# Performance work log

Hardware: AMD Instinct MI355X
Metric: run time of the kernel (lower is better)

The kernel has to match this reference:

```python
import jax, jax.numpy as jnp
import numpy as np

D_MODEL = 768
D_ATTN = 768
D_LLM = 4096
N_HEADS = 12
HEAD_DIM = D_ATTN // N_HEADS


def setup_inputs() -> dict:
    key = jax.random.key(0)
    ks = jax.random.split(key, 11)
    B, L, S = 8, 1024, 1000
    inp = {
        "target_embedding": jax.random.normal(ks[0], (B, L, D_MODEL), jnp.float32),
        "source_embedding": jax.random.normal(ks[1], (S, D_LLM), jnp.float32),
        "value_embedding": jax.random.normal(ks[2], (S, D_LLM), jnp.float32),
        # nn.Linear params: y = x @ W.T + b, W shape (out, in)
        "Wq": jax.random.normal(ks[3], (D_ATTN, D_MODEL), jnp.float32) * (1.0 / np.sqrt(D_MODEL)),
        "bq": jax.random.normal(ks[4], (D_ATTN,), jnp.float32) * 0.02,
        "Wk": jax.random.normal(ks[5], (D_ATTN, D_LLM), jnp.float32) * (1.0 / np.sqrt(D_LLM)),
        "bk": jax.random.normal(ks[6], (D_ATTN,), jnp.float32) * 0.02,
        "Wv": jax.random.normal(ks[7], (D_ATTN, D_LLM), jnp.float32) * (1.0 / np.sqrt(D_LLM)),
        "bv": jax.random.normal(ks[8], (D_ATTN,), jnp.float32) * 0.02,
        "Wo": jax.random.normal(ks[9], (D_LLM, D_ATTN), jnp.float32) * (1.0 / np.sqrt(D_ATTN)),
        "bo": jax.random.normal(ks[10], (D_LLM,), jnp.float32) * 0.02,
    }
    return inp


def reference(target_embedding, source_embedding, value_embedding,
              Wq, bq, Wk, bk, Wv, bv, Wo, bo):
    B, L, _ = target_embedding.shape
    S, _ = source_embedding.shape
    H, E = N_HEADS, HEAD_DIM
    scale = E ** -0.5

    q = (target_embedding @ Wq.T + bq).reshape(B, L, H, E)   # (B,L,H,E)
    k = (source_embedding @ Wk.T + bk).reshape(S, H, E)      # (S,H,E) shared KV
    v = (value_embedding @ Wv.T + bv).reshape(S, H, E)

    scores = jnp.einsum('blhe,she->bhls', q, k) * scale      # (B,H,L,S)
    A = jax.nn.softmax(scores, axis=-1)                      # dropout inactive (eval)
    rep = jnp.einsum('bhls,she->blhe', A, v).reshape(B, L, D_ATTN)
    return rep @ Wo.T + bo                                   # (B,L,D_LLM)
```

## Files before the change

### kernel.cpp

```cpp
#include <hip/hip_runtime.h>

typedef __attribute__((ext_vector_type(8))) short short8;
typedef __attribute__((ext_vector_type(4))) short short4v;
typedef __attribute__((ext_vector_type(4))) float f32x4;

#define DEVI __device__ __forceinline__

DEVI unsigned short f2bf(float x) {
  unsigned u = __builtin_bit_cast(unsigned, x);
  u += 0x7fff + ((u >> 16) & 1u);
  return (unsigned short)(u >> 16);
}

template <int MODE, int WM, int WN>
DEVI void proj_body(const float* __restrict__ A, const float* __restrict__ W,
                    const float* __restrict__ bias, void* __restrict__ outp,
                    int M, int K, int ldo, float scale,
                    int bm, int bn, int kbeg, int kend) {
  constexpr int TM = WM * 32, TN = WN * 32, TR = TM + TN;
  __shared__ unsigned short sAB[TR][40];
  const int tid  = threadIdx.x;
  const int lane = tid & 63, wid = tid >> 6;
  const int wr = (wid >> 1) * (WM * 16), wc = (wid & 1) * (WN * 16);
  const int m0 = bm * TM, n0 = bn * TN;
  const int srow = tid >> 3;
  const int scol = (tid & 7) * 4;
  const int lr = lane & 15, lk = (lane >> 4) * 8;

  f32x4 acc[WM][WN];
#pragma unroll
  for (int i = 0; i < WM; ++i)
#pragma unroll
    for (int j = 0; j < WN; ++j) acc[i][j] = (f32x4){0.f, 0.f, 0.f, 0.f};

  for (int k0 = kbeg; k0 < kend; k0 += 32) {
#pragma unroll
    for (int p = 0; p < TR / 32; ++p) {
      const int row = p * 32 + srow;
      f32x4 t;
      if (row < TM) {
        const int rg = m0 + row;
        t = (rg < M) ? *(const f32x4*)(A + (size_t)rg * K + k0 + scol)
                     : (f32x4){0.f, 0.f, 0.f, 0.f};
      } else {
        t = *(const f32x4*)(W + (size_t)(n0 + row - TM) * K + k0 + scol);
      }
      short4v s;
#pragma unroll
      for (int j = 0; j < 4; ++j) s[j] = (short)f2bf(t[j]);
      *(short4v*)&sAB[row][scol] = s;
    }
    __syncthreads();
    short8 af[WM], bfr[WN];
#pragma unroll
    for (int i = 0; i < WM; ++i) af[i]  = *(const short8*)&sAB[wr + i * 16 + lr][lk];
#pragma unroll
    for (int j = 0; j < WN; ++j) bfr[j] = *(const short8*)&sAB[TM + wc + j * 16 + lr][lk];
#pragma unroll
    for (int i = 0; i < WM; ++i)
#pragma unroll
      for (int j = 0; j < WN; ++j)
        acc[i][j] = __builtin_amdgcn_mfma_f32_16x16x32_bf16(af[i], bfr[j], acc[i][j], 0, 0, 0);
    __syncthreads();
  }

#pragma unroll
  for (int i = 0; i < WM; ++i) {
#pragma unroll
    for (int j = 0; j < WN; ++j) {
      const int n  = n0 + wc + j * 16 + lr;
      const int mb = m0 + wr + i * 16 + (lane >> 4) * 4;
      if (MODE == 0) {
        const float bv = bias[n];
        unsigned short* out = (unsigned short*)outp;
#pragma unroll
        for (int r = 0; r < 4; ++r)
          out[(size_t)(mb + r) * ldo + n] = f2bf((acc[i][j][r] + bv) * scale);
      } else {
        float* out = (float*)outp;
#pragma unroll
        for (int r = 0; r < 4; ++r)
          atomicAdd(&out[(size_t)(mb + r) * ldo + n], acc[i][j][r]);
      }
    }
  }
}

__global__ __launch_bounds__(256) void qproj_kernel(const float* __restrict__ target,
                                                    const float* __restrict__ Wq,
                                                    const float* __restrict__ bq,
                                                    unsigned short* __restrict__ qb) {
  proj_body<0, 2, 4>(target, Wq, bq, qb, 8192, 768, 768, 0.125f,
                     blockIdx.x, blockIdx.y, 0, 768);
}

__global__ __launch_bounds__(256) void kvproj_kernel(const float* __restrict__ source,
                                                     const float* __restrict__ value,
                                                     const float* __restrict__ Wk,
                                                     const float* __restrict__ Wv,
                                                     float* __restrict__ kacc,
                                                     float* __restrict__ vacc) {
  const int kv = blockIdx.z >> 3, ks = blockIdx.z & 7;
  const float* A = kv ? value : source;
  const float* W = kv ? Wv : Wk;
  float* out = kv ? vacc : kacc;
  proj_body<2, 2, 4>(A, W, nullptr, out, 1000, 4096, 768, 1.0f,
                     blockIdx.x, blockIdx.y, ks * 512, ks * 512 + 512);
}

__global__ __launch_bounds__(256) void finalize_kv(const float* __restrict__ kacc,
                                                   const float* __restrict__ vacc,
                                                   const float* __restrict__ bk,
                                                   const float* __restrict__ bv,
                                                   unsigned short* __restrict__ kb,
                                                   unsigned short* __restrict__ vtb) {
  if (blockIdx.z == 0) {
    const int i = (blockIdx.x * 256 + threadIdx.x) * 8;
    const int col = i % 768;
    short8 p;
#pragma unroll
    for (int j = 0; j < 8; ++j) p[j] = (short)f2bf(kacc[i + j] + bk[col + j]);
    *(short8*)&kb[i] = p;
  } else {
    const int idx = blockIdx.x * 256 + threadIdx.x;
    const int n = idx >> 7;
    const int s0 = (idx & 127) * 8;
    const float bvn = bv[n];
    short8 p;
#pragma unroll
    for (int j = 0; j < 8; ++j) p[j] = (short)f2bf(vacc[(size_t)(s0 + j) * 768 + n] + bvn);
    *(short8*)&vtb[(size_t)n * 1024 + s0] = p;
  }
}

__global__ __launch_bounds__(256) void attn_kernel(const unsigned short* __restrict__ q,
                                                   const unsigned short* __restrict__ k,
                                                   const unsigned short* __restrict__ vt,
                                                   unsigned short* __restrict__ rep) {
  __shared__ unsigned short sK[64][72];
  __shared__ unsigned short sV[64][72];
  __shared__ unsigned short sP[128][72];

  const int tid = threadIdx.x;
  const int lane = tid & 63, w = tid >> 6;
  const int q0 = blockIdx.x * 128;
  const int b = blockIdx.y / 12, h = blockIdx.y % 12;
  const int lr = lane & 15, lk = (lane >> 4) * 8;
  const int qrow_base = b * 1024 + q0 + w * 32;

  short8 qf[2][2];
#pragma unroll
  for (int fm = 0; fm < 2; ++fm)
#pragma unroll
    for (int kk = 0; kk < 2; ++kk)
      qf[fm][kk] = *(const short8*)&q[(size_t)(qrow_base + fm * 16 + lr) * 768 + h * 64 + kk * 32 + lk];

  float m_run[2][4], l_run[2][4];
  f32x4 o[2][4];
#pragma unroll
  for (int fm = 0; fm < 2; ++fm)
#pragma unroll
    for (int r = 0; r < 4; ++r) {
      m_run[fm][r] = -1e30f;
      l_run[fm][r] = 0.f;
    }
#pragma unroll
  for (int fm = 0; fm < 2; ++fm)
#pragma unroll
    for (int je = 0; je < 4; ++je) o[fm][je] = (f32x4){0.f, 0.f, 0.f, 0.f};

  const int strow = tid >> 2;
  const int stc = (tid & 3) * 16;

  for (int t = 0; t < 16; ++t) {
    const int s0 = t * 64;
    __syncthreads();
    {
      const unsigned short* ks = &k[(size_t)(s0 + strow) * 768 + h * 64 + stc];
      *(short8*)&sK[strow][stc]     = *(const short8*)ks;
      *(short8*)&sK[strow][stc + 8] = *(const short8*)(ks + 8);
      const unsigned short* vs = &vt[(size_t)(h * 64 + strow) * 1024 + s0 + stc];
      *(short8*)&sV[strow][stc]     = *(const short8*)vs;
      *(short8*)&sV[strow][stc + 8] = *(const short8*)(vs + 8);
    }
    __syncthreads();

    f32x4 sc_acc[2][4];
#pragma unroll
    for (int fm = 0; fm < 2; ++fm)
#pragma unroll
      for (int j = 0; j < 4; ++j) sc_acc[fm][j] = (f32x4){0.f, 0.f, 0.f, 0.f};
    short8 kf[4][2];
#pragma unroll
    for (int j = 0; j < 4; ++j)
#pragma unroll
      for (int kk = 0; kk < 2; ++kk)
        kf[j][kk] = *(const short8*)&sK[j * 16 + lr][kk * 32 + lk];
#pragma unroll
    for (int fm = 0; fm < 2; ++fm)
#pragma unroll
      for (int j = 0; j < 4; ++j)
#pragma unroll
        for (int kk = 0; kk < 2; ++kk)
          sc_acc[fm][j] = __builtin_amdgcn_mfma_f32_16x16x32_bf16(qf[fm][kk], kf[j][kk], sc_acc[fm][j], 0, 0, 0);

    if (s0 + 64 > 1000) {
#pragma unroll
      for (int j = 0; j < 4; ++j)
        if (s0 + j * 16 + lr >= 1000) {
#pragma unroll
          for (int fm = 0; fm < 2; ++fm)
#pragma unroll
            for (int r = 0; r < 4; ++r) sc_acc[fm][j][r] = -1e30f;
        }
    }

#pragma unroll
    for (int fm = 0; fm < 2; ++fm) {
#pragma unroll
      for (int r = 0; r < 4; ++r) {
        float mx = fmaxf(fmaxf(sc_acc[fm][0][r], sc_acc[fm][1][r]),
                         fmaxf(sc_acc[fm][2][r], sc_acc[fm][3][r]));
#pragma unroll
        for (int d = 1; d < 16; d <<= 1) mx = fmaxf(mx, __shfl_xor(mx, d));
        const float mnew = fmaxf(m_run[fm][r], mx);
        const float fac = __expf(m_run[fm][r] - mnew);
        m_run[fm][r] = mnew;
        float rs = 0.f;
#pragma unroll
        for (int j = 0; j < 4; ++j) {
          const float p = __expf(sc_acc[fm][j][r] - mnew);
          sc_acc[fm][j][r] = p;
          rs += p;
        }
#pragma unroll
        for (int d = 1; d < 16; d <<= 1) rs += __shfl_xor(rs, d);
        l_run[fm][r] = l_run[fm][r] * fac + rs;
#pragma unroll
        for (int je = 0; je < 4; ++je) o[fm][je][r] *= fac;
      }
    }

#pragma unroll
    for (int fm = 0; fm < 2; ++fm)
#pragma unroll
      for (int j = 0; j < 4; ++j)
#pragma unroll
        for (int r = 0; r < 4; ++r)
          sP[w * 32 + fm * 16 + (lane >> 4) * 4 + r][j * 16 + lr] = f2bf(sc_acc[fm][j][r]);
    asm volatile("s_waitcnt lgkmcnt(0)" ::: "memory");

    short8 pf[2][2], vf[4][2];
#pragma unroll
    for (int fm = 0; fm < 2; ++fm)
#pragma unroll
      for (int kk = 0; kk < 2; ++kk)
        pf[fm][kk] = *(const short8*)&sP[w * 32 + fm * 16 + lr][kk * 32 + lk];
#pragma unroll
    for (int je = 0; je < 4; ++je)
#pragma unroll
      for (int kk = 0; kk < 2; ++kk)
        vf[je][kk] = *(const short8*)&sV[je * 16 + lr][kk * 32 + lk];
#pragma unroll
    for (int fm = 0; fm < 2; ++fm)
#pragma unroll
      for (int je = 0; je < 4; ++je)
#pragma unroll
        for (int kk = 0; kk < 2; ++kk)
          o[fm][je] = __builtin_amdgcn_mfma_f32_16x16x32_bf16(pf[fm][kk], vf[je][kk], o[fm][je], 0, 0, 0);
  }

  float inv_l[2][4];
#pragma unroll
  for (int fm = 0; fm < 2; ++fm)
#pragma unroll
    for (int r = 0; r < 4; ++r) inv_l[fm][r] = 1.0f / l_run[fm][r];
#pragma unroll
  for (int fm = 0; fm < 2; ++fm)
#pragma unroll
    for (int je = 0; je < 4; ++je)
#pragma unroll
      for (int r = 0; r < 4; ++r)
        sP[w * 32 + fm * 16 + (lane >> 4) * 4 + r][je * 16 + lr] = f2bf(o[fm][je][r] * inv_l[fm][r]);
  __syncthreads();
  const int orow = tid >> 1, oc = (tid & 1) * 32;
  unsigned short* dst = &rep[(size_t)(b * 1024 + q0 + orow) * 768 + h * 64 + oc];
#pragma unroll
  for (int i = 0; i < 4; ++i)
    *(short8*)(dst + i * 8) = *(const short8*)&sP[orow][oc + i * 8];
}

__global__ __launch_bounds__(256) void oproj_kernel(const unsigned short* __restrict__ A,
                                                    const unsigned short* __restrict__ B,
                                                    const float* __restrict__ bo,
                                                    float* __restrict__ out) {
  __shared__ unsigned short sA[4096];
  __shared__ unsigned short sB[4096];
  const int tid = threadIdx.x;
  const int lane = tid & 63, wid = tid >> 6;
  const int wr = (wid >> 1) * 64, wc = (wid & 1) * 64;
  const int m0 = blockIdx.x * 128, n0 = blockIdx.y * 128;
  const int grow = lane >> 2;
  const int gcol = (lane & 3) * 8;
  const int lr = lane & 15, lk = (lane >> 4) * 8;

  f32x4 acc[4][4];
#pragma unroll
  for (int i = 0; i < 4; ++i)
#pragma unroll
    for (int j = 0; j < 4; ++j) acc[i][j] = (f32x4){0.f, 0.f, 0.f, 0.f};

  for (int k0 = 0; k0 < 768; k0 += 32) {
#pragma unroll
    for (int jj = 0; jj < 2; ++jj) {
      const int chunk = wid * 2 + jj;
      const int row = chunk * 16 + grow;
      __builtin_amdgcn_global_load_lds(
          (const __attribute__((address_space(1))) unsigned int*)(A + (size_t)(m0 + row) * 768 + k0 + gcol),
          (__attribute__((address_space(3))) unsigned int*)(sA + chunk * 512),
          16, 0, 0);
      __builtin_amdgcn_global_load_lds(
          (const __attribute__((address_space(1))) unsigned int*)(B + (size_t)(n0 + row) * 768 + k0 + gcol),
          (__attribute__((address_space(3))) unsigned int*)(sB + chunk * 512),
          16, 0, 0);
    }
    __syncthreads();
    short8 af[4], bfr[4];
#pragma unroll
    for (int i = 0; i < 4; ++i) af[i]  = *(const short8*)&sA[(wr + i * 16 + lr) * 32 + lk];
#pragma unroll
    for (int j = 0; j < 4; ++j) bfr[j] = *(const short8*)&sB[(wc + j * 16 + lr) * 32 + lk];
#pragma unroll
    for (int i = 0; i < 4; ++i)
#pragma unroll
      for (int j = 0; j < 4; ++j)
        acc[i][j] = __builtin_amdgcn_mfma_f32_16x16x32_bf16(af[i], bfr[j], acc[i][j], 0, 0, 0);
    __syncthreads();
  }

#pragma unroll
  for (int i = 0; i < 4; ++i) {
#pragma unroll
    for (int j = 0; j < 4; ++j) {
      const int n = n0 + wc + j * 16 + lr;
      const float bv = bo[n];
      const int mb = m0 + wr + i * 16 + (lane >> 4) * 4;
#pragma unroll
      for (int r = 0; r < 4; ++r)
        out[(size_t)(mb + r) * 4096 + n] = acc[i][j][r] + bv;
    }
  }
}

__global__ __launch_bounds__(256) void cvt_kernel(const float* __restrict__ in,
                                                  unsigned short* __restrict__ out) {
  const size_t i = ((size_t)blockIdx.x * 256 + threadIdx.x) * 8;
  f32x4 a = *(const f32x4*)(in + i);
  f32x4 b = *(const f32x4*)(in + i + 4);
  short8 p;
#pragma unroll
  for (int j = 0; j < 4; ++j) p[j] = (short)f2bf(a[j]);
#pragma unroll
  for (int j = 0; j < 4; ++j) p[j + 4] = (short)f2bf(b[j]);
  *(short8*)&out[i] = p;
}

extern "C" void kernel_launch(void* const* d_in, const int* in_sizes, int n_in,
                              void* d_out, int out_size, void* d_ws, size_t ws_size,
                              hipStream_t stream) {
  const float* target = (const float*)d_in[0];
  const float* source = (const float*)d_in[1];
  const float* value  = (const float*)d_in[2];
  const float* Wq = (const float*)d_in[3];
  const float* bq = (const float*)d_in[4];
  const float* Wk = (const float*)d_in[5];
  const float* bk = (const float*)d_in[6];
  const float* Wv = (const float*)d_in[7];
  const float* bv = (const float*)d_in[8];
  const float* Wo = (const float*)d_in[9];
  const float* bo = (const float*)d_in[10];
  float* out = (float*)d_out;

  char* ws = (char*)d_ws;
  unsigned short* qb   = (unsigned short*)(ws);
  unsigned short* kb   = (unsigned short*)(ws + 12582912);
  unsigned short* vtb  = (unsigned short*)(ws + 14155776);
  unsigned short* repb = (unsigned short*)(ws + 15728640);
  unsigned short* wob  = (unsigned short*)(ws + 28311552);
  float* kacc = (float*)(ws + 34603008);
  float* vacc = (float*)(ws + 37748736);

  hipMemsetAsync(ws + 34603008, 0, 6291456, stream);

  cvt_kernel<<<1536, 256, 0, stream>>>(Wo, wob);
  qproj_kernel<<<dim3(128, 6), 256, 0, stream>>>(target, Wq, bq, qb);
  kvproj_kernel<<<dim3(16, 6, 16), 256, 0, stream>>>(source, value, Wk, Wv, kacc, vacc);
  finalize_kv<<<dim3(384, 1, 2), 256, 0, stream>>>(kacc, vacc, bk, bv, kb, vtb);
  attn_kernel<<<dim3(8, 96), 256, 0, stream>>>(qb, kb, vtb, repb);
  oproj_kernel<<<dim3(64, 32), 256, 0, stream>>>(repb, wob, bo, out);
}
```

Before: 521.1 us.

## Pre-convert all inputs to bf16, unify GEMMs, drop atomics, streamline softmax

Adds one kernel that converts every fp32 input and weight to bf16, staging the results in the output buffer as scratch. All projections then share a single bf16 GEMM body that loads tiles with direct global-to-LDS loads. The K/V split-K projection now writes partial sums to separate buffers that finalize_kv adds up, which removes the atomics and the memset. The attention kernel swaps the MFMA operands so each lane owns score columns, uses exp2 with the log2e factor folded into the Q scale, and cuts shuffle reductions per row. The trade-off is an extra full pass over the large inputs for conversion, plus output-buffer reuse that depends on oproj running last.

```diff
diff --git a/kernel.cpp b/kernel.cpp
--- a/kernel.cpp
+++ b/kernel.cpp
@@ -1,8 +1,8 @@
 #include <hip/hip_runtime.h>
 
 typedef __attribute__((ext_vector_type(8))) short short8;
-typedef __attribute__((ext_vector_type(4))) short short4v;
 typedef __attribute__((ext_vector_type(4))) float f32x4;
+typedef __attribute__((ext_vector_type(2))) unsigned u32x2;
 
 #define DEVI __device__ __forceinline__
 
@@ -12,54 +12,93 @@
   return (unsigned short)(u >> 16);
 }
 
-template <int MODE, int WM, int WN>
-DEVI void proj_body(const float* __restrict__ A, const float* __restrict__ W,
+DEVI unsigned pkbf2(float a, float b) {
+  return (unsigned)f2bf(a) | ((unsigned)f2bf(b) << 16);
+}
+
+__global__ __launch_bounds__(256) void cvt_all(
+    const float* __restrict__ t0, const float* __restrict__ t1,
+    const float* __restrict__ t2, const float* __restrict__ t3,
+    const float* __restrict__ t4, const float* __restrict__ t5,
+    const float* __restrict__ t6,
+    unsigned short* __restrict__ o0, unsigned short* __restrict__ o1,
+    unsigned short* __restrict__ o2, unsigned short* __restrict__ o3,
+    unsigned short* __restrict__ o4, unsigned short* __restrict__ o5,
+    unsigned short* __restrict__ o6) {
+  const unsigned gid = blockIdx.x * 256 + threadIdx.x;
+  const float* src;
+  unsigned short* dst;
+  unsigned base;
+  if (gid < 786432u)       { src = t0; dst = o0; base = 0u; }
+  else if (gid < 1298432u) { src = t1; dst = o1; base = 786432u; }
+  else if (gid < 1810432u) { src = t2; dst = o2; base = 1298432u; }
+  else if (gid < 1884160u) { src = t3; dst = o3; base = 1810432u; }
+  else if (gid < 2277376u) { src = t4; dst = o4; base = 1884160u; }
+  else if (gid < 2670592u) { src = t5; dst = o5; base = 2277376u; }
+  else                     { src = t6; dst = o6; base = 2670592u; }
+  const size_t i = (size_t)(gid - base) * 8;
+  f32x4 a = *(const f32x4*)(src + i);
+  f32x4 b = *(const f32x4*)(src + i + 4);
+  short8 p;
+#pragma unroll
+  for (int j = 0; j < 4; ++j) p[j] = (short)f2bf(a[j]);
+#pragma unroll
+  for (int j = 0; j < 4; ++j) p[j + 4] = (short)f2bf(b[j]);
+  *(short8*)&dst[i] = p;
+}
+
+template <int TM, int MODE>
+DEVI void gemm_body(const unsigned short* __restrict__ A,
+                    const unsigned short* __restrict__ B,
                     const float* __restrict__ bias, void* __restrict__ outp,
-                    int M, int K, int ldo, float scale,
+                    int M, int lda, int ldo, float scale,
                     int bm, int bn, int kbeg, int kend) {
-  constexpr int TM = WM * 32, TN = WN * 32, TR = TM + TN;
-  __shared__ unsigned short sAB[TR][40];
-  const int tid  = threadIdx.x;
+  constexpr int WM = TM / 32;
+  constexpr int ROWS = TM + 128;
+  constexpr int NCH = ROWS / 16;
+  constexpr int CPW = NCH / 4;
+  __shared__ unsigned short sAB[ROWS * 32];
+  const int tid = threadIdx.x;
   const int lane = tid & 63, wid = tid >> 6;
-  const int wr = (wid >> 1) * (WM * 16), wc = (wid & 1) * (WN * 16);
-  const int m0 = bm * TM, n0 = bn * TN;
-  const int srow = tid >> 3;
-  const int scol = (tid & 7) * 4;
+  const int wr = (wid >> 1) * (WM * 16), wc = (wid & 1) * 64;
+  const int m0 = bm * TM, n0 = bn * 128;
+  const int grow = lane >> 2, gcol = (lane & 3) * 8;
   const int lr = lane & 15, lk = (lane >> 4) * 8;
 
-  f32x4 acc[WM][WN];
+  f32x4 acc[WM][4];
 #pragma unroll
   for (int i = 0; i < WM; ++i)
 #pragma unroll
-    for (int j = 0; j < WN; ++j) acc[i][j] = (f32x4){0.f, 0.f, 0.f, 0.f};
+    for (int j = 0; j < 4; ++j) acc[i][j] = (f32x4){0.f, 0.f, 0.f, 0.f};
 
   for (int k0 = kbeg; k0 < kend; k0 += 32) {
 #pragma unroll
-    for (int p = 0; p < TR / 32; ++p) {
-      const int row = p * 32 + srow;
-      f32x4 t;
-      if (row < TM) {
-        const int rg = m0 + row;
-        t = (rg < M) ? *(const f32x4*)(A + (size_t)rg * K + k0 + scol)
-                     : (f32x4){0.f, 0.f, 0.f, 0.f};
+    for (int i = 0; i < CPW; ++i) {
+      const int c = wid * CPW + i;
+      const int row = c * 16 + grow;
+      const unsigned short* src;
+      if (c * 16 < TM) {
+        int rg = m0 + row;
+        if (rg > M - 1) rg = M - 1;
+        src = A + (size_t)rg * lda + k0 + gcol;
       } else {
-        t = *(const f32x4*)(W + (size_t)(n0 + row - TM) * K + k0 + scol);
+        src = B + (size_t)(n0 + row - TM) * lda + k0 + gcol;
       }
-      short4v s;
-#pragma unroll
-      for (int j = 0; j < 4; ++j) s[j] = (short)f2bf(t[j]);
-      *(short4v*)&sAB[row][scol] = s;
+      __builtin_amdgcn_global_load_lds(
+          (const __attribute__((address_space(1))) unsigned int*)src,
+          (__attribute__((address_space(3))) unsigned int*)(sAB + c * 512),
+          16, 0, 0);
     }
     __syncthreads();
-    short8 af[WM], bfr[WN];
-#pragma unroll
-    for (int i = 0; i < WM; ++i) af[i]  = *(const short8*)&sAB[wr + i * 16 + lr][lk];
-#pragma unroll
-    for (int j = 0; j < WN; ++j) bfr[j] = *(const short8*)&sAB[TM + wc + j * 16 + lr][lk];
+    short8 af[WM], bfr[4];
+#pragma unroll
+    for (int i = 0; i < WM; ++i) af[i]  = *(const short8*)&sAB[(wr + i * 16 + lr) * 32 + lk];
+#pragma unroll
+    for (int j = 0; j < 4; ++j)  bfr[j] = *(const short8*)&sAB[(TM + wc + j * 16 + lr) * 32 + lk];
 #pragma unroll
     for (int i = 0; i < WM; ++i)
 #pragma unroll
-      for (int j = 0; j < WN; ++j)
+      for (int j = 0; j < 4; ++j)
         acc[i][j] = __builtin_amdgcn_mfma_f32_16x16x32_bf16(af[i], bfr[j], acc[i][j], 0, 0, 0);
     __syncthreads();
   }
@@ -67,7 +106,7 @@
 #pragma unroll
   for (int i = 0; i < WM; ++i) {
 #pragma unroll
-    for (int j = 0; j < WN; ++j) {
+    for (int j = 0; j < 4; ++j) {
       const int n  = n0 + wc + j * 16 + lr;
       const int mb = m0 + wr + i * 16 + (lane >> 4) * 4;
       if (MODE == 0) {
@@ -76,40 +115,52 @@
 #pragma unroll
         for (int r = 0; r < 4; ++r)
           out[(size_t)(mb + r) * ldo + n] = f2bf((acc[i][j][r] + bv) * scale);
+      } else if (MODE == 1) {
+        const float bv = bias[n];
+        float* out = (float*)outp;
+#pragma unroll
+        for (int r = 0; r < 4; ++r)
+          out[(size_t)(mb + r) * ldo + n] = acc[i][j][r] + bv;
       } else {
         float* out = (float*)outp;
 #pragma unroll
         for (int r = 0; r < 4; ++r)
-          atomicAdd(&out[(size_t)(mb + r) * ldo + n], acc[i][j][r]);
+          out[(size_t)(mb + r) * ldo + n] = acc[i][j][r];
       }
     }
   }
 }
 
-__global__ __launch_bounds__(256) void qproj_kernel(const float* __restrict__ target,
-                                                    const float* __restrict__ Wq,
+__global__ __launch_bounds__(256) void qproj_kernel(const unsigned short* __restrict__ A,
+                                                    const unsigned short* __restrict__ B,
                                                     const float* __restrict__ bq,
                                                     unsigned short* __restrict__ qb) {
-  proj_body<0, 2, 4>(target, Wq, bq, qb, 8192, 768, 768, 0.125f,
-                     blockIdx.x, blockIdx.y, 0, 768);
-}
-
-__global__ __launch_bounds__(256) void kvproj_kernel(const float* __restrict__ source,
-                                                     const float* __restrict__ value,
-                                                     const float* __restrict__ Wk,
-                                                     const float* __restrict__ Wv,
-                                                     float* __restrict__ kacc,
-                                                     float* __restrict__ vacc) {
-  const int kv = blockIdx.z >> 3, ks = blockIdx.z & 7;
-  const float* A = kv ? value : source;
-  const float* W = kv ? Wv : Wk;
-  float* out = kv ? vacc : kacc;
-  proj_body<2, 2, 4>(A, W, nullptr, out, 1000, 4096, 768, 1.0f,
-                     blockIdx.x, blockIdx.y, ks * 512, ks * 512 + 512);
-}
-
-__global__ __launch_bounds__(256) void finalize_kv(const float* __restrict__ kacc,
-                                                   const float* __restrict__ vacc,
+  gemm_body<64, 0>(A, B, bq, qb, 8192, 768, 768, 0.18033688011112042f,
+                   blockIdx.x, blockIdx.y, 0, 768);
+}
+
+__global__ __launch_bounds__(256) void kvproj_kernel(const unsigned short* __restrict__ sb,
+                                                     const unsigned short* __restrict__ vb,
+                                                     const unsigned short* __restrict__ wkb,
+                                                     const unsigned short* __restrict__ wvb,
+                                                     float* __restrict__ parts) {
+  const int mat = blockIdx.z >> 2, ks = blockIdx.z & 3;
+  const unsigned short* A = mat ? vb : sb;
+  const unsigned short* B = mat ? wvb : wkb;
+  float* out = parts + (size_t)blockIdx.z * 786432;
+  gemm_body<64, 2>(A, B, nullptr, out, 1000, 4096, 768, 1.0f,
+                   blockIdx.x, blockIdx.y, ks * 1024, ks * 1024 + 1024);
+}
+
+__global__ __launch_bounds__(256) void oproj_kernel(const unsigned short* __restrict__ A,
+                                                    const unsigned short* __restrict__ B,
+                                                    const float* __restrict__ bo,
+                                                    float* __restrict__ out) {
+  gemm_body<128, 1>(A, B, bo, out, 8192, 768, 4096, 1.0f,
+                    blockIdx.x, blockIdx.y, 0, 768);
+}
+
+__global__ __launch_bounds__(256) void finalize_kv(const float* __restrict__ parts,
                                                    const float* __restrict__ bk,
                                                    const float* __restrict__ bv,
                                                    unsigned short* __restrict__ kb,
@@ -117,19 +168,33 @@
   if (blockIdx.z == 0) {
     const int i = (blockIdx.x * 256 + threadIdx.x) * 8;
     const int col = i % 768;
-    short8 p;
-#pragma unroll
-    for (int j = 0; j < 8; ++j) p[j] = (short)f2bf(kacc[i + j] + bk[col + j]);
-    *(short8*)&kb[i] = p;
+    f32x4 sa = (f32x4){0.f, 0.f, 0.f, 0.f}, sb = sa;
+#pragma unroll
+    for (int p = 0; p < 4; ++p) {
+      sa += *(const f32x4*)(parts + (size_t)p * 786432 + i);
+      sb += *(const f32x4*)(parts + (size_t)p * 786432 + i + 4);
+    }
+    short8 o;
+#pragma unroll
+    for (int j = 0; j < 4; ++j) o[j] = (short)f2bf(sa[j] + bk[col + j]);
+#pragma unroll
+    for (int j = 0; j < 4; ++j) o[j + 4] = (short)f2bf(sb[j] + bk[col + 4 + j]);
+    *(short8*)&kb[i] = o;
   } else {
     const int idx = blockIdx.x * 256 + threadIdx.x;
     const int n = idx >> 7;
     const int s0 = (idx & 127) * 8;
     const float bvn = bv[n];
-    short8 p;
-#pragma unroll
-    for (int j = 0; j < 8; ++j) p[j] = (short)f2bf(vacc[(size_t)(s0 + j) * 768 + n] + bvn);
-    *(short8*)&vtb[(size_t)n * 1024 + s0] = p;
+    short8 o;
+#pragma unroll
+    for (int j = 0; j < 8; ++j) {
+      float s = 0.f;
+#pragma unroll
+      for (int p = 0; p < 4; ++p)
+        s += parts[(size_t)(4 + p) * 786432 + (size_t)(s0 + j) * 768 + n];
+      o[j] = (short)f2bf(s + bvn);
+    }
+    *(short8*)&vtb[(size_t)n * 1024 + s0] = o;
   }
 }
 
@@ -143,9 +208,10 @@
 
   const int tid = threadIdx.x;
   const int lane = tid & 63, w = tid >> 6;
+  const int g = lane >> 4;
   const int q0 = blockIdx.x * 128;
   const int b = blockIdx.y / 12, h = blockIdx.y % 12;
-  const int lr = lane & 15, lk = (lane >> 4) * 8;
+  const int lr = lane & 15, lk = g * 8;
   const int qrow_base = b * 1024 + q0 + w * 32;
 
   short8 qf[2][2];
@@ -155,22 +221,15 @@
     for (int kk = 0; kk < 2; ++kk)
       qf[fm][kk] = *(const short8*)&q[(size_t)(qrow_base + fm * 16 + lr) * 768 + h * 64 + kk * 32 + lk];
 
-  float m_run[2][4], l_run[2][4];
+  float m_run[2] = {-1e30f, -1e30f};
+  float l_run[2] = {0.f, 0.f};
   f32x4 o[2][4];
 #pragma unroll
   for (int fm = 0; fm < 2; ++fm)
 #pragma unroll
-    for (int r = 0; r < 4; ++r) {
-      m_run[fm][r] = -1e30f;
-      l_run[fm][r] = 0.f;
-    }
-#pragma unroll
-  for (int fm = 0; fm < 2; ++fm)
-#pragma unroll
     for (int je = 0; je < 4; ++je) o[fm][je] = (f32x4){0.f, 0.f, 0.f, 0.f};
 
-  const int strow = tid >> 2;
-  const int stc = (tid & 3) * 16;
+  const int strow = tid >> 2, stc = (tid & 3) * 16;
 
   for (int t = 0; t < 16; ++t) {
     const int s0 = t * 64;
@@ -185,11 +244,11 @@
     }
     __syncthreads();
 
-    f32x4 sc_acc[2][4];
-#pragma unroll
-    for (int fm = 0; fm < 2; ++fm)
-#pragma unroll
-      for (int j = 0; j < 4; ++j) sc_acc[fm][j] = (f32x4){0.f, 0.f, 0.f, 0.f};
+    f32x4 sc[2][4];
+#pragma unroll
+    for (int fm = 0; fm < 2; ++fm)
+#pragma unroll
+      for (int j = 0; j < 4; ++j) sc[fm][j] = (f32x4){0.f, 0.f, 0.f, 0.f};
     short8 kf[4][2];
 #pragma unroll
     for (int j = 0; j < 4; ++j)
@@ -202,52 +261,66 @@
       for (int j = 0; j < 4; ++j)
 #pragma unroll
         for (int kk = 0; kk < 2; ++kk)
-          sc_acc[fm][j] = __builtin_amdgcn_mfma_f32_16x16x32_bf16(qf[fm][kk], kf[j][kk], sc_acc[fm][j], 0, 0, 0);
+          sc[fm][j] = __builtin_amdgcn_mfma_f32_16x16x32_bf16(kf[j][kk], qf[fm][kk], sc[fm][j], 0, 0, 0);
 
     if (s0 + 64 > 1000) {
 #pragma unroll
       for (int j = 0; j < 4; ++j)
-        if (s0 + j * 16 + lr >= 1000) {
-#pragma unroll
-          for (int fm = 0; fm < 2; ++fm)
-#pragma unroll
-            for (int r = 0; r < 4; ++r) sc_acc[fm][j][r] = -1e30f;
-        }
-    }
-
+#pragma unroll
+        for (int r = 0; r < 4; ++r)
+          if (s0 + j * 16 + g * 4 + r >= 1000) {
+            sc[0][j][r] = -1e30f;
+            sc[1][j][r] = -1e30f;
+          }
+    }
+
+    float fac[2];
 #pragma unroll
     for (int fm = 0; fm < 2; ++fm) {
-#pragma unroll
-      for (int r = 0; r < 4; ++r) {
-        float mx = fmaxf(fmaxf(sc_acc[fm][0][r], sc_acc[fm][1][r]),
-                         fmaxf(sc_acc[fm][2][r], sc_acc[fm][3][r]));
-#pragma unroll
-        for (int d = 1; d < 16; d <<= 1) mx = fmaxf(mx, __shfl_xor(mx, d));
-        const float mnew = fmaxf(m_run[fm][r], mx);
-        const float fac = __expf(m_run[fm][r] - mnew);
-        m_run[fm][r] = mnew;
-        float rs = 0.f;
-#pragma unroll
-        for (int j = 0; j < 4; ++j) {
-          const float p = __expf(sc_acc[fm][j][r] - mnew);
-          sc_acc[fm][j][r] = p;
+      float mx = -1e30f;
+#pragma unroll
+      for (int j = 0; j < 4; ++j) {
+        float a = fmaxf(fmaxf(sc[fm][j][0], sc[fm][j][1]),
+                        fmaxf(sc[fm][j][2], sc[fm][j][3]));
+        mx = fmaxf(mx, a);
+      }
+      mx = fmaxf(mx, __shfl_xor(mx, 16));
+      mx = fmaxf(mx, __shfl_xor(mx, 32));
+      const float mnew = fmaxf(m_run[fm], mx);
+      fac[fm] = exp2f(m_run[fm] - mnew);
+      m_run[fm] = mnew;
+      float rs = 0.f;
+#pragma unroll
+      for (int j = 0; j < 4; ++j)
+#pragma unroll
+        for (int r = 0; r < 4; ++r) {
+          const float p = exp2f(sc[fm][j][r] - mnew);
+          sc[fm][j][r] = p;
           rs += p;
         }
-#pragma unroll
-        for (int d = 1; d < 16; d <<= 1) rs += __shfl_xor(rs, d);
-        l_run[fm][r] = l_run[fm][r] * fac + rs;
-#pragma unroll
-        for (int je = 0; je < 4; ++je) o[fm][je][r] *= fac;
+      rs += __shfl_xor(rs, 16);
+      rs += __shfl_xor(rs, 32);
+      l_run[fm] = l_run[fm] * fac[fm] + rs;
+    }
+
+#pragma unroll
+    for (int fm = 0; fm < 2; ++fm)
+#pragma unroll
+      for (int r = 0; r < 4; ++r) {
+        const float fq = __shfl(fac[fm], g * 20 + r);
+#pragma unroll
+        for (int je = 0; je < 4; ++je) o[fm][je][r] *= fq;
       }
-    }
-
-#pragma unroll
-    for (int fm = 0; fm < 2; ++fm)
-#pragma unroll
-      for (int j = 0; j < 4; ++j)
-#pragma unroll
-        for (int r = 0; r < 4; ++r)
-          sP[w * 32 + fm * 16 + (lane >> 4) * 4 + r][j * 16 + lr] = f2bf(sc_acc[fm][j][r]);
+
+#pragma unroll
+    for (int fm = 0; fm < 2; ++fm)
+#pragma unroll
+      for (int j = 0; j < 4; ++j) {
+        u32x2 pw;
+        pw[0] = pkbf2(sc[fm][j][0], sc[fm][j][1]);
+        pw[1] = pkbf2(sc[fm][j][2], sc[fm][j][3]);
+        *(u32x2*)&sP[w * 32 + fm * 16 + lr][j * 16 + g * 4] = pw;
+      }
     asm volatile("s_waitcnt lgkmcnt(0)" ::: "memory");
 
     short8 pf[2][2], vf[4][2];
@@ -270,99 +343,23 @@
           o[fm][je] = __builtin_amdgcn_mfma_f32_16x16x32_bf16(pf[fm][kk], vf[je][kk], o[fm][je], 0, 0, 0);
   }
 
-  float inv_l[2][4];
-#pragma unroll
-  for (int fm = 0; fm < 2; ++fm)
-#pragma unroll
-    for (int r = 0; r < 4; ++r) inv_l[fm][r] = 1.0f / l_run[fm][r];
-#pragma unroll
-  for (int fm = 0; fm < 2; ++fm)
-#pragma unroll
-    for (int je = 0; je < 4; ++je)
-#pragma unroll
-      for (int r = 0; r < 4; ++r)
-        sP[w * 32 + fm * 16 + (lane >> 4) * 4 + r][je * 16 + lr] = f2bf(o[fm][je][r] * inv_l[fm][r]);
+#pragma unroll
+  for (int fm = 0; fm < 2; ++fm) {
+    const float il = 1.0f / l_run[fm];
+#pragma unroll
+    for (int r = 0; r < 4; ++r) {
+      const float iq = __shfl(il, g * 20 + r);
+#pragma unroll
+      for (int je = 0; je < 4; ++je)
+        sP[w * 32 + fm * 16 + g * 4 + r][je * 16 + lr] = f2bf(o[fm][je][r] * iq);
+    }
+  }
   __syncthreads();
   const int orow = tid >> 1, oc = (tid & 1) * 32;
   unsigned short* dst = &rep[(size_t)(b * 1024 + q0 + orow) * 768 + h * 64 + oc];
 #pragma unroll
   for (int i = 0; i < 4; ++i)
     *(short8*)(dst + i * 8) = *(const short8*)&sP[orow][oc + i * 8];
-}
-
-__global__ __launch_bounds__(256) void oproj_kernel(const unsigned short* __restrict__ A,
-                                                    const unsigned short* __restrict__ B,
-                                                    const float* __restrict__ bo,
-                                                    float* __restrict__ out) {
-  __shared__ unsigned short sA[4096];
-  __shared__ unsigned short sB[4096];
-  const int tid = threadIdx.x;
-  const int lane = tid & 63, wid = tid >> 6;
-  const int wr = (wid >> 1) * 64, wc = (wid & 1) * 64;
-  const int m0 = blockIdx.x * 128, n0 = blockIdx.y * 128;
-  const int grow = lane >> 2;
-  const int gcol = (lane & 3) * 8;
-  const int lr = lane & 15, lk = (lane >> 4) * 8;
-
-  f32x4 acc[4][4];
-#pragma unroll
-  for (int i = 0; i < 4; ++i)
-#pragma unroll
-    for (int j = 0; j < 4; ++j) acc[i][j] = (f32x4){0.f, 0.f, 0.f, 0.f};
-
-  for (int k0 = 0; k0 < 768; k0 += 32) {
-#pragma unroll
-    for (int jj = 0; jj < 2; ++jj) {
-      const int chunk = wid * 2 + jj;
-      const int row = chunk * 16 + grow;
-      __builtin_amdgcn_global_load_lds(
-          (const __attribute__((address_space(1))) unsigned int*)(A + (size_t)(m0 + row) * 768 + k0 + gcol),
-          (__attribute__((address_space(3))) unsigned int*)(sA + chunk * 512),
-          16, 0, 0);
-      __builtin_amdgcn_global_load_lds(
-          (const __attribute__((address_space(1))) unsigned int*)(B + (size_t)(n0 + row) * 768 + k0 + gcol),
-          (__attribute__((address_space(3))) unsigned int*)(sB + chunk * 512),
-          16, 0, 0);
-    }
-    __syncthreads();
-    short8 af[4], bfr[4];
-#pragma unroll
-    for (int i = 0; i < 4; ++i) af[i]  = *(const short8*)&sA[(wr + i * 16 + lr) * 32 + lk];
-#pragma unroll
-    for (int j = 0; j < 4; ++j) bfr[j] = *(const short8*)&sB[(wc + j * 16 + lr) * 32 + lk];
-#pragma unroll
-    for (int i = 0; i < 4; ++i)
-#pragma unroll
-      for (int j = 0; j < 4; ++j)
-        acc[i][j] = __builtin_amdgcn_mfma_f32_16x16x32_bf16(af[i], bfr[j], acc[i][j], 0, 0, 0);
-    __syncthreads();
-  }
-
-#pragma unroll
-  for (int i = 0; i < 4; ++i) {
-#pragma unroll
-    for (int j = 0; j < 4; ++j) {
-      const int n = n0 + wc + j * 16 + lr;
-      const float bv = bo[n];
-      const int mb = m0 + wr + i * 16 + (lane >> 4) * 4;
-#pragma unroll
-      for (int r = 0; r < 4; ++r)
-        out[(size_t)(mb + r) * 4096 + n] = acc[i][j][r] + bv;
-    }
-  }
-}
-
-__global__ __launch_bounds__(256) void cvt_kernel(const float* __restrict__ in,
-                                                  unsigned short* __restrict__ out) {
-  const size_t i = ((size_t)blockIdx.x * 256 + threadIdx.x) * 8;
-  f32x4 a = *(const f32x4*)(in + i);
-  f32x4 b = *(const f32x4*)(in + i + 4);
-  short8 p;
-#pragma unroll
-  for (int j = 0; j < 4; ++j) p[j] = (short)f2bf(a[j]);
-#pragma unroll
-  for (int j = 0; j < 4; ++j) p[j + 4] = (short)f2bf(b[j]);
-  *(short8*)&out[i] = p;
 }
 
 extern "C" void kernel_launch(void* const* d_in, const int* in_sizes, int n_in,
@@ -387,15 +384,21 @@
   unsigned short* vtb  = (unsigned short*)(ws + 14155776);
   unsigned short* repb = (unsigned short*)(ws + 15728640);
   unsigned short* wob  = (unsigned short*)(ws + 28311552);
-  float* kacc = (float*)(ws + 34603008);
-  float* vacc = (float*)(ws + 37748736);
-
-  hipMemsetAsync(ws + 34603008, 0, 6291456, stream);
-
-  cvt_kernel<<<1536, 256, 0, stream>>>(Wo, wob);
-  qproj_kernel<<<dim3(128, 6), 256, 0, stream>>>(target, Wq, bq, qb);
-  kvproj_kernel<<<dim3(16, 6, 16), 256, 0, stream>>>(source, value, Wk, Wv, kacc, vacc);
-  finalize_kv<<<dim3(384, 1, 2), 256, 0, stream>>>(kacc, vacc, bk, bv, kb, vtb);
+
+  char* ob = (char*)d_out;
+  unsigned short* targetb = (unsigned short*)(ob);
+  unsigned short* sourceb = (unsigned short*)(ob + 12582912);
+  unsigned short* valueb  = (unsigned short*)(ob + 20774912);
+  unsigned short* wqb     = (unsigned short*)(ob + 28966912);
+  unsigned short* wkb     = (unsigned short*)(ob + 30146560);
+  unsigned short* wvb     = (unsigned short*)(ob + 36438016);
+  float* parts            = (float*)(ob + 42729472);
+
+  cvt_all<<<11968, 256, 0, stream>>>(target, source, value, Wq, Wk, Wv, Wo,
+                                     targetb, sourceb, valueb, wqb, wkb, wvb, wob);
+  qproj_kernel<<<dim3(128, 6), 256, 0, stream>>>(targetb, wqb, bq, qb);
+  kvproj_kernel<<<dim3(16, 6, 8), 256, 0, stream>>>(sourceb, valueb, wkb, wvb, parts);
+  finalize_kv<<<dim3(384, 1, 2), 256, 0, stream>>>(parts, bk, bv, kb, vtb);
   attn_kernel<<<dim3(8, 96), 256, 0, stream>>>(qb, kb, vtb, repb);
   oproj_kernel<<<dim3(64, 32), 256, 0, stream>>>(repb, wob, bo, out);
 }
```

Result: faster. 448.2 us (-14.0%).
